# Kernel tuning notes

Measured on AMD Instinct MI355X. Metric: run time of the kernel, lower is better.

The kernel has to match this reference:

```python
import jax, jax.numpy as jnp
import numpy as np

D = 1024
B, S_IMG, S_CTX = 2, 4096, 512
EPS = 1e-6


def rmsnorm(x, eps=1e-6):
    return x * jax.lax.rsqrt(jnp.mean(x * x, axis=-1, keepdims=True) + eps)


def layernorm(x, eps=1e-6):
    mu = jnp.mean(x, axis=-1, keepdims=True)
    var = jnp.mean((x - mu) ** 2, axis=-1, keepdims=True)
    return (x - mu) * jax.lax.rsqrt(var + eps)


def act_quant(x):
    # per-token 8-bit absmax quant
    scale = 127.0 / jnp.clip(jnp.max(jnp.abs(x), axis=-1, keepdims=True), 1e-5)
    return jnp.clip(jnp.round(x * scale), -128, 127) / scale


def weight_quant(w):
    # ternary (1.58-bit) absmean quant
    scale = 1.0 / jnp.clip(jnp.mean(jnp.abs(w)), 1e-5)
    return jnp.clip(jnp.round(w * scale), -1, 1) / scale


def bitlinear(x, w):
    # BitNet: RMSNorm -> STE activation quant, STE ternary weight quant
    xn = rmsnorm(x)
    xq = xn + jax.lax.stop_gradient(act_quant(xn) - xn)
    wq = w + jax.lax.stop_gradient(weight_quant(w) - w)
    return jnp.einsum('bsd,od->bso', xq, wq)


def ada_ln_zero(x, emb, w, b):
    e = (jax.nn.silu(emb) @ w.T + b)[:, None, :]  # [B,1,6D]
    scale_msa, shift_msa, gate_msa, scale_mlp, shift_mlp, gate_mlp = jnp.split(e, 6, axis=2)
    xn = layernorm(x) * (1.0 + scale_msa) + shift_msa
    return xn, gate_msa, shift_mlp, scale_mlp, gate_mlp


def hgrn_bit_attention(x, wi, wf, wg, wo, gnorm_w):
    i = bitlinear(x, wi)
    f = jax.nn.sigmoid(bitlinear(x, wf))
    i = jax.nn.silu(i) * (1.0 - f)  # swiglu(i, 1-f)
    # elementwise linear recurrence h_t = f_t * h_{t-1} + i_t over seq dim
    def step(h, xs):
        i_t, f_t = xs
        h = f_t * h + i_t
        return h, h
    _, o = jax.lax.scan(step, jnp.zeros_like(i[:, 0]), (i.transpose(1, 0, 2), f.transpose(1, 0, 2)))
    o = o.transpose(1, 0, 2)  # [B,S,D]
    g = bitlinear(x, wg)
    o = rmsnorm(o) * gnorm_w * (g * jax.nn.sigmoid(g))  # RMSNorm + swish gate
    return bitlinear(o, wo)


def bit_mlp(x, w_gate, w_down):
    y = bitlinear(x, w_gate)
    gate, y = jnp.split(y, 2, axis=-1)
    return bitlinear(jax.nn.silu(gate) * y, w_down)


def flux_block(hidden_states, encoder_hidden_states, temb,
               adaln_w, adaln_b, adaln_ctx_w, adaln_ctx_b,
               attn_wi, attn_wf, attn_wg, attn_wo, attn_gnorm_w,
               ff_wgate, ff_wdown, ffc_wgate, ffc_wdown):
    nh, gate_msa, shift_mlp, scale_mlp, gate_mlp = ada_ln_zero(hidden_states, temb, adaln_w, adaln_b)
    nc, c_gate_msa, c_shift_mlp, c_scale_mlp, c_gate_mlp = ada_ln_zero(encoder_hidden_states, temb, adaln_ctx_w, adaln_ctx_b)
    len_c = nc.shape[1]
    joint = jnp.concatenate([nc, nh], axis=1)
    attn_out = hgrn_bit_attention(joint, attn_wi, attn_wf, attn_wg, attn_wo, attn_gnorm_w)
    c_attn, x_attn = attn_out[:, :len_c], attn_out[:, len_c:]

    hidden_states = hidden_states + gate_msa * x_attn
    nh2 = layernorm(hidden_states) * (1.0 + scale_mlp) + shift_mlp
    hidden_states = hidden_states + gate_mlp * bit_mlp(nh2, ff_wgate, ff_wdown)

    encoder_hidden_states = encoder_hidden_states + c_gate_msa * c_attn
    nc2 = layernorm(encoder_hidden_states) * (1.0 + c_scale_mlp) + c_shift_mlp
    encoder_hidden_states = encoder_hidden_states + c_gate_mlp * bit_mlp(nc2, ffc_wgate, ffc_wdown)
    return hidden_states, encoder_hidden_states


def setup_inputs() -> dict:
    key = jax.random.key(0)
    ks = jax.random.split(key, 16)
    w = lambda k, shape: jax.random.normal(k, shape, jnp.float32) * 0.02
    return {
        'hidden_states': jax.random.normal(ks[0], (B, S_IMG, D), jnp.float32),
        'encoder_hidden_states': jax.random.normal(ks[1], (B, S_CTX, D), jnp.float32),
        'temb': jax.random.normal(ks[2], (B, D), jnp.float32),
        'adaln_w': w(ks[3], (6 * D, D)), 'adaln_b': jnp.zeros((6 * D,), jnp.float32),
        'adaln_ctx_w': w(ks[4], (6 * D, D)), 'adaln_ctx_b': jnp.zeros((6 * D,), jnp.float32),
        'attn_wi': w(ks[5], (D, D)), 'attn_wf': w(ks[6], (D, D)),
        'attn_wg': w(ks[7], (D, D)), 'attn_wo': w(ks[8], (D, D)),
        'attn_gnorm_w': jnp.ones((D,), jnp.float32),
        'ff_wgate': w(ks[9], (8 * D, D)), 'ff_wdown': w(ks[10], (D, 4 * D)),
        'ffc_wgate': w(ks[11], (8 * D, D)), 'ffc_wdown': w(ks[12], (D, 4 * D)),
    }


def reference(hidden_states, encoder_hidden_states, temb,
              adaln_w, adaln_b, adaln_ctx_w, adaln_ctx_b,
              attn_wi, attn_wf, attn_wg, attn_wo, attn_gnorm_w,
              ff_wgate, ff_wdown, ffc_wgate, ffc_wdown):
    return flux_block(hidden_states, encoder_hidden_states, temb,
                      adaln_w, adaln_b, adaln_ctx_w, adaln_ctx_b,
                      attn_wi, attn_wf, attn_wg, attn_wo, attn_gnorm_w,
                      ff_wgate, ff_wdown, ffc_wgate, ffc_wdown)
```

## Files before the change

### kernel.cpp

```cpp
#include <hip/hip_runtime.h>
#include <hip/hip_bf16.h>
#include <stdint.h>

#define DM   1024
#define SJ   4608
#define SCTX 512
#define SIMG 4096
#define NCH  512
#define TCH  9

typedef __attribute__((ext_vector_type(4))) int   i32x4;
typedef __attribute__((ext_vector_type(4))) float f32x4;

__device__ __forceinline__ float bf2f(unsigned short u){
  union { unsigned int i; float f; } v; v.i = ((unsigned int)u) << 16; return v.f;
}
__device__ __forceinline__ unsigned short f2bf(float f){
  unsigned int u = __float_as_uint(f);
  u += 0x7fffu + ((u >> 16) & 1u);
  return (unsigned short)(u >> 16);
}
__device__ __forceinline__ float sigm(float x){ return 1.f/(1.f+__expf(-x)); }
__device__ __forceinline__ signed char q8(float v, float lo, float hi){
  return (signed char)(int)fminf(fmaxf(rintf(v),lo),hi);
}

__device__ __forceinline__ float wsum(float v){
  #pragma unroll
  for(int o=32;o>0;o>>=1) v += __shfl_xor(v,o);
  return v;
}
__device__ __forceinline__ float wmax(float v){
  #pragma unroll
  for(int o=32;o>0;o>>=1) v = fmaxf(v,__shfl_xor(v,o));
  return v;
}
__device__ __forceinline__ void blockSumSum(float& a, float& b, float* s1, float* s2){
  a = wsum(a); b = wsum(b);
  if(!(threadIdx.x&63)){ s1[threadIdx.x>>6]=a; s2[threadIdx.x>>6]=b; }
  __syncthreads();
  a = s1[0]+s1[1]+s1[2]+s1[3];
  b = s2[0]+s2[1]+s2[2]+s2[3];
  __syncthreads();
}
__device__ __forceinline__ void blockSumMax(float& a, float& b, float* s1, float* s2){
  a = wsum(a); b = wmax(b);
  if(!(threadIdx.x&63)){ s1[threadIdx.x>>6]=a; s2[threadIdx.x>>6]=b; }
  __syncthreads();
  a = s1[0]+s1[1]+s1[2]+s1[3];
  b = fmaxf(fmaxf(s2[0],s2[1]),fmaxf(s2[2],s2[3]));
  __syncthreads();
}

typedef __attribute__((address_space(1))) void gvoid_t;
typedef __attribute__((address_space(3))) void lvoid_t;
__device__ __forceinline__ void gl_lds16(const void* g, void* l){
  __builtin_amdgcn_global_load_lds((gvoid_t*)g, (lvoid_t*)l, 16, 0, 0);
}

struct WList {
  const float* w[8];
  unsigned long long n[8];
  signed char* q[8];
};

__global__ __launch_bounds__(256)
void wq_reduce(WList L, float* __restrict__ part){
  __shared__ float s1[4];
  int m = blockIdx.y;
  const float4* w4 = (const float4*)L.w[m];
  size_t n4 = L.n[m] >> 2;
  float s = 0.f;
  for(size_t i = (size_t)blockIdx.x*256 + threadIdx.x; i < n4; i += (size_t)512*256){
    float4 v = w4[i];
    s += fabsf(v.x)+fabsf(v.y)+fabsf(v.z)+fabsf(v.w);
  }
  s = wsum(s);
  if(!(threadIdx.x&63)) s1[threadIdx.x>>6] = s;
  __syncthreads();
  if(!threadIdx.x) part[m*512 + blockIdx.x] = s1[0]+s1[1]+s1[2]+s1[3];
}

__global__ __launch_bounds__(256)
void wq_finalize(WList L, const float* __restrict__ part, float* __restrict__ swinv){
  __shared__ float s1[4];
  int m = blockIdx.x;
  float s = part[m*512 + threadIdx.x] + part[m*512 + 256 + threadIdx.x];
  s = wsum(s);
  if(!(threadIdx.x&63)) s1[threadIdx.x>>6] = s;
  __syncthreads();
  if(!threadIdx.x){
    float mean = (s1[0]+s1[1]+s1[2]+s1[3]) / (float)L.n[m];
    swinv[m] = fmaxf(mean, 1e-5f);
  }
}

__global__ __launch_bounds__(256)
void wq_quant(WList L, const float* __restrict__ swinv){
  int m = blockIdx.y;
  float sc = 1.f / swinv[m];
  const float4* w4 = (const float4*)L.w[m];
  signed char* q = L.q[m];
  size_t n4 = L.n[m] >> 2;
  for(size_t i = (size_t)blockIdx.x*256 + threadIdx.x; i < n4; i += (size_t)1024*256){
    float4 v = w4[i];
    char4 o;
    o.x = q8(v.x*sc,-1.f,1.f);
    o.y = q8(v.y*sc,-1.f,1.f);
    o.z = q8(v.z*sc,-1.f,1.f);
    o.w = q8(v.w*sc,-1.f,1.f);
    ((char4*)q)[i] = o;
  }
}

__global__ __launch_bounds__(256)
void adaln_gemv(const float* __restrict__ temb, const float* __restrict__ W,
                const float* __restrict__ bias, float* __restrict__ e){
  int o = blockIdx.x*4 + (threadIdx.x>>6);
  int b = blockIdx.y;
  int lane = threadIdx.x & 63;
  const float4* t4 = (const float4*)(temb + b*DM);
  const float4* w4 = (const float4*)(W + (size_t)o*DM);
  float acc = 0.f;
  #pragma unroll
  for(int i=0;i<4;i++){
    float4 tv = t4[i*64+lane], wv = w4[i*64+lane];
    acc += (tv.x*sigm(tv.x))*wv.x + (tv.y*sigm(tv.y))*wv.y
         + (tv.z*sigm(tv.z))*wv.z + (tv.w*sigm(tv.w))*wv.w;
  }
  acc = wsum(acc);
  if(!lane) e[b*6144 + o] = acc + bias[o];
}

__global__ __launch_bounds__(256)
void modnorm_quant(const float* __restrict__ x, int bshift,
                   const float* __restrict__ e, int scaleOff, int shiftOff,
                   signed char* __restrict__ xq, float* __restrict__ rsx,
                   int outRowOff, int outBatchStride){
  __shared__ float s1[4], s2[4];
  const int tid = threadIdx.x;
  const int row = blockIdx.x;
  const int b = row >> bshift, s = row & ((1<<bshift)-1);
  float4 xv = ((const float4*)(x + (size_t)row*DM))[tid];
  float sum = xv.x+xv.y+xv.z+xv.w;
  float ss  = xv.x*xv.x+xv.y*xv.y+xv.z*xv.z+xv.w*xv.w;
  blockSumSum(sum, ss, s1, s2);
  float mu  = sum * (1.f/DM);
  float inv = rsqrtf(ss*(1.f/DM) - mu*mu + 1e-6f);
  float4 scv = ((const float4*)(e + b*6144 + scaleOff))[tid];
  float4 shv = ((const float4*)(e + b*6144 + shiftOff))[tid];
  float n0 = (xv.x-mu)*inv*(1.f+scv.x)+shv.x;
  float n1 = (xv.y-mu)*inv*(1.f+scv.y)+shv.y;
  float n2 = (xv.z-mu)*inv*(1.f+scv.z)+shv.z;
  float n3 = (xv.w-mu)*inv*(1.f+scv.w)+shv.w;
  float ss2 = n0*n0+n1*n1+n2*n2+n3*n3;
  float mx  = fmaxf(fmaxf(fabsf(n0),fabsf(n1)),fmaxf(fabsf(n2),fabsf(n3)));
  blockSumMax(ss2, mx, s1, s2);
  float rms   = rsqrtf(ss2*(1.f/DM) + 1e-6f);
  float amaxn = fmaxf(mx*rms, 1e-5f);
  float k     = rms*127.f/amaxn;
  int orow = b*outBatchStride + outRowOff + s;
  char4 q;
  q.x = q8(n0*k,-128.f,127.f);
  q.y = q8(n1*k,-128.f,127.f);
  q.z = q8(n2*k,-128.f,127.f);
  q.w = q8(n3*k,-128.f,127.f);
  ((char4*)(xq + (size_t)orow*DM))[tid] = q;
  if(!tid) rsx[orow] = amaxn*(1.f/127.f);
}

__global__ __launch_bounds__(256)
void resid_modnorm(const float* __restrict__ x, const unsigned short* __restrict__ attn,
                   int attnRowOff, int bshift,
                   const float* __restrict__ e,
                   float* __restrict__ hout,
                   signed char* __restrict__ xq, float* __restrict__ rsx){
  __shared__ float s1[4], s2[4];
  const int tid = threadIdx.x;
  const int row = blockIdx.x;
  const int b = row >> bshift, s = row & ((1<<bshift)-1);
  const int arow = b*SJ + attnRowOff + s;
  float4 xv = ((const float4*)(x + (size_t)row*DM))[tid];
  ushort4 av = ((const ushort4*)(attn + (size_t)arow*DM))[tid];
  float4 gv = ((const float4*)(e + b*6144 + 2*1024))[tid];
  float h0 = xv.x + gv.x*bf2f(av.x);
  float h1 = xv.y + gv.y*bf2f(av.y);
  float h2 = xv.z + gv.z*bf2f(av.z);
  float h3 = xv.w + gv.w*bf2f(av.w);
  ((float4*)(hout + (size_t)row*DM))[tid] = make_float4(h0,h1,h2,h3);
  float sum = h0+h1+h2+h3;
  float ss  = h0*h0+h1*h1+h2*h2+h3*h3;
  blockSumSum(sum, ss, s1, s2);
  float mu  = sum * (1.f/DM);
  float inv = rsqrtf(ss*(1.f/DM) - mu*mu + 1e-6f);
  float4 scv = ((const float4*)(e + b*6144 + 3*1024))[tid];
  float4 shv = ((const float4*)(e + b*6144 + 4*1024))[tid];
  float n0 = (h0-mu)*inv*(1.f+scv.x)+shv.x;
  float n1 = (h1-mu)*inv*(1.f+scv.y)+shv.y;
  float n2 = (h2-mu)*inv*(1.f+scv.z)+shv.z;
  float n3 = (h3-mu)*inv*(1.f+scv.w)+shv.w;
  float ss2 = n0*n0+n1*n1+n2*n2+n3*n3;
  float mx  = fmaxf(fmaxf(fabsf(n0),fabsf(n1)),fmaxf(fabsf(n2),fabsf(n3)));
  blockSumMax(ss2, mx, s1, s2);
  float rms   = rsqrtf(ss2*(1.f/DM) + 1e-6f);
  float amaxn = fmaxf(mx*rms, 1e-5f);
  float k     = rms*127.f/amaxn;
  char4 q;
  q.x = q8(n0*k,-128.f,127.f);
  q.y = q8(n1*k,-128.f,127.f);
  q.z = q8(n2*k,-128.f,127.f);
  q.w = q8(n3*k,-128.f,127.f);
  ((char4*)(xq + (size_t)row*DM))[tid] = q;
  if(!tid) rsx[row] = amaxn*(1.f/127.f);
}

__global__ __launch_bounds__(256)
void resid_out(const float* __restrict__ hnew, const unsigned short* __restrict__ mlp,
               const float* __restrict__ e, int bshift, float* __restrict__ out){
  const int tid = threadIdx.x;
  const int row = blockIdx.x;
  const int b = row >> bshift;
  float4 hv = ((const float4*)(hnew + (size_t)row*DM))[tid];
  ushort4 mv = ((const ushort4*)(mlp + (size_t)row*DM))[tid];
  float4 gv = ((const float4*)(e + b*6144 + 5*1024))[tid];
  float4 o;
  o.x = hv.x + gv.x*bf2f(mv.x);
  o.y = hv.y + gv.y*bf2f(mv.y);
  o.z = hv.z + gv.z*bf2f(mv.z);
  o.w = hv.w + gv.w*bf2f(mv.w);
  ((float4*)(out + (size_t)row*DM))[tid] = o;
}

__global__ __launch_bounds__(256)
void rmsq4096(const unsigned short* __restrict__ z, signed char* __restrict__ zq,
              float* __restrict__ rsx){
  __shared__ float s1[4], s2[4];
  const int tid = threadIdx.x;
  const unsigned short* zr = z + (size_t)blockIdx.x*4096;
  signed char* qr = zq + (size_t)blockIdx.x*4096;
  float v[16];
  #pragma unroll
  for(int i=0;i<4;i++){
    ushort4 u = ((const ushort4*)zr)[tid + i*256];
    v[i*4+0]=bf2f(u.x); v[i*4+1]=bf2f(u.y); v[i*4+2]=bf2f(u.z); v[i*4+3]=bf2f(u.w);
  }
  float ss=0.f, mx=0.f;
  #pragma unroll
  for(int i=0;i<16;i++){ ss += v[i]*v[i]; mx = fmaxf(mx, fabsf(v[i])); }
  blockSumMax(ss, mx, s1, s2);
  float rms   = rsqrtf(ss*(1.f/4096.f) + 1e-6f);
  float amaxn = fmaxf(mx*rms, 1e-5f);
  float k     = rms*127.f/amaxn;
  #pragma unroll
  for(int i=0;i<4;i++){
    char4 q;
    q.x = q8(v[i*4+0]*k,-128.f,127.f);
    q.y = q8(v[i*4+1]*k,-128.f,127.f);
    q.z = q8(v[i*4+2]*k,-128.f,127.f);
    q.w = q8(v[i*4+3]*k,-128.f,127.f);
    ((char4*)qr)[tid + i*256] = q;
  }
  if(!tid) rsx[blockIdx.x] = amaxn*(1.f/127.f);
}

__global__ __launch_bounds__(256)
void scan_pass1(const unsigned short* __restrict__ ir, const unsigned short* __restrict__ fr,
                float* __restrict__ A, float* __restrict__ B){
  int c = blockIdx.x, b = blockIdx.y;
  int d0 = threadIdx.x*4;
  size_t base = ((size_t)b*SJ + (size_t)c*TCH)*DM + d0;
  float a0=1,a1=1,a2=1,a3=1, h0=0,h1=0,h2=0,h3=0;
  #pragma unroll
  for(int t=0;t<TCH;t++){
    ushort4 iv = *(const ushort4*)(ir + base + (size_t)t*DM);
    ushort4 fv = *(const ushort4*)(fr + base + (size_t)t*DM);
    float f0=sigm(bf2f(fv.x)), f1=sigm(bf2f(fv.y)), f2=sigm(bf2f(fv.z)), f3=sigm(bf2f(fv.w));
    float x0=bf2f(iv.x), x1=bf2f(iv.y), x2=bf2f(iv.z), x3=bf2f(iv.w);
    float p0=x0*sigm(x0)*(1.f-f0), p1=x1*sigm(x1)*(1.f-f1);
    float p2=x2*sigm(x2)*(1.f-f2), p3=x3*sigm(x3)*(1.f-f3);
    h0=f0*h0+p0; h1=f1*h1+p1; h2=f2*h2+p2; h3=f3*h3+p3;
    a0*=f0; a1*=f1; a2*=f2; a3*=f3;
  }
  size_t idx = (size_t)c*2048 + b*1024 + d0;
  *(float4*)(A + idx) = make_float4(a0,a1,a2,a3);
  *(float4*)(B + idx) = make_float4(h0,h1,h2,h3);
}

__global__ __launch_bounds__(256)
void scan_pass2(const float* __restrict__ A, const float* __restrict__ B, float* __restrict__ H){
  int chain = blockIdx.x*256 + threadIdx.x;
  float h = 0.f;
  for(int c0=0;c0<NCH;c0+=8){
    float a[8], bb[8];
    #pragma unroll
    for(int u=0;u<8;u++){
      a[u]  = A[(size_t)(c0+u)*2048 + chain];
      bb[u] = B[(size_t)(c0+u)*2048 + chain];
    }
    #pragma unroll
    for(int u=0;u<8;u++){
      H[(size_t)(c0+u)*2048 + chain] = h;
      h = a[u]*h + bb[u];
    }
  }
}

__global__ __launch_bounds__(256)
void scan3_gnorm(const unsigned short* __restrict__ ir, const unsigned short* __restrict__ fr,
                 const float* __restrict__ H, const unsigned short* __restrict__ g,
                 const float* __restrict__ gnw,
                 signed char* __restrict__ xq, float* __restrict__ rsx){
  __shared__ float s1[4], s2[4];
  int c = blockIdx.x, b = blockIdx.y;
  const int tid = threadIdx.x;
  int d0 = tid*4;
  size_t base = ((size_t)b*SJ + (size_t)c*TCH)*DM + d0;
  float4 hv = *(const float4*)(H + (size_t)c*2048 + b*1024 + d0);
  float h0=hv.x, h1=hv.y, h2=hv.z, h3=hv.w;
  float4 wv = ((const float4*)gnw)[tid];
  #pragma unroll
  for(int t=0;t<TCH;t++){
    ushort4 iv = *(const ushort4*)(ir + base + (size_t)t*DM);
    ushort4 fv = *(const ushort4*)(fr + base + (size_t)t*DM);
    float f0=sigm(bf2f(fv.x)), f1=sigm(bf2f(fv.y)), f2=sigm(bf2f(fv.z)), f3=sigm(bf2f(fv.w));
    float x0=bf2f(iv.x), x1=bf2f(iv.y), x2=bf2f(iv.z), x3=bf2f(iv.w);
    float p0=x0*sigm(x0)*(1.f-f0), p1=x1*sigm(x1)*(1.f-f1);
    float p2=x2*sigm(x2)*(1.f-f2), p3=x3*sigm(x3)*(1.f-f3);
    h0=f0*h0+p0; h1=f1*h1+p1; h2=f2*h2+p2; h3=f3*h3+p3;
    float ss = h0*h0+h1*h1+h2*h2+h3*h3, dummy = 0.f;
    blockSumSum(ss, dummy, s1, s2);
    float rms = rsqrtf(ss*(1.f/DM) + 1e-6f);
    ushort4 gv = *(const ushort4*)(g + base + (size_t)t*DM);
    float g0=bf2f(gv.x), g1=bf2f(gv.y), g2=bf2f(gv.z), g3=bf2f(gv.w);
    float n0 = h0*rms*wv.x*(g0*sigm(g0));
    float n1 = h1*rms*wv.y*(g1*sigm(g1));
    float n2 = h2*rms*wv.z*(g2*sigm(g2));
    float n3 = h3*rms*wv.w*(g3*sigm(g3));
    float ss2 = n0*n0+n1*n1+n2*n2+n3*n3;
    float mx  = fmaxf(fmaxf(fabsf(n0),fabsf(n1)),fmaxf(fabsf(n2),fabsf(n3)));
    blockSumMax(ss2, mx, s1, s2);
    float rms2  = rsqrtf(ss2*(1.f/DM) + 1e-6f);
    float amaxn = fmaxf(mx*rms2, 1e-5f);
    float k     = rms2*127.f/amaxn;
    char4 q;
    q.x = q8(n0*k,-128.f,127.f);
    q.y = q8(n1*k,-128.f,127.f);
    q.z = q8(n2*k,-128.f,127.f);
    q.w = q8(n3*k,-128.f,127.f);
    size_t row = (size_t)b*SJ + (size_t)c*TCH + t;
    *(char4*)(xq + row*DM + d0) = q;
    if(!tid) rsx[row] = amaxn*(1.f/127.f);
  }
}

#define EPI_IFG    0
#define EPI_OUT    1
#define EPI_GLU    2

struct GemmP {
  const float* rsx;
  const float* swinv;
  unsigned short* outb;
  float* outf;
  const float* egate;
  int bshift;
  const signed char* w2;
};

template<int VAR, int EPI, int SWZ>
__global__ __launch_bounds__(512, 2)
void gemm8(const signed char* __restrict__ Aq, const signed char* __restrict__ Bq,
           int Ncols, int K, int lda, GemmP p){
  constexpr int BBYT = (VAR==2)? 16384 : 32768;
  constexpr int TB   = 32768 + BBYT;
  constexpr int NF   = (VAR==0)? 4 : 2;
  constexpr int BN   = (VAR==0)? 256 : 128;
  __shared__ char lds[2*TB];

  const int tid = threadIdx.x, wv = tid>>6, lane = tid&63;
  const int wm = wv>>2, wn = wv&3;
  const int nwg = gridDim.x*gridDim.y;
  const int id  = blockIdx.y*gridDim.x + blockIdx.x;
  int nb, mb;
  if constexpr (SWZ==1){
    const int x = id&7, j = id>>3;
    nb = x*4 + (j&3);
    mb = j>>2;
  } else {
    const int wg = (id&7)*(nwg>>3) + (id>>3);
    nb = wg % gridDim.x; mb = wg / gridDim.x;
  }

  const int srow = wv*8 + (lane>>3);
  const int sch  = ((lane&7) ^ (lane>>3))*16;
  const signed char* ag  = Aq + (size_t)(mb*256 + srow)*lda + sch;
  const signed char* bg1 = Bq + (size_t)(nb*BN  + srow)*lda + sch;
  const signed char* bg2 = nullptr;
  if constexpr (VAR==1) bg2 = p.w2 + (size_t)(nb*128 + srow)*lda + sch;
  const int wvoff = wv*1024;

  auto stageA = [&](char* bufn, int rb, int k0){
    gl_lds16(ag + (size_t)rb*lda + k0, bufn + rb*128 + wvoff);
  };
  auto stageB = [&](char* bufn, int rb, int k0, int m2){
    const signed char* src = m2 ? bg2 : bg1;
    gl_lds16(src + (size_t)rb*lda + k0, bufn + 32768 + m2*16384 + rb*128 + wvoff);
  };
  auto stagePh = [&](int ph, char* bufn, int kn){
    if constexpr (VAR==0){
      if(ph==0){ stageB(bufn,0,kn,0);   stageB(bufn,64,kn,0); }
      else if(ph==1){ stageB(bufn,128,kn,0); stageB(bufn,192,kn,0); }
      else if(ph==2){ stageA(bufn,0,kn);   stageA(bufn,128,kn); }
      else          { stageA(bufn,64,kn);  stageA(bufn,192,kn); }
    } else if constexpr (VAR==1){
      if(ph==0){ stageB(bufn,0,kn,0);  stageB(bufn,64,kn,0); }
      else if(ph==1){ stageB(bufn,0,kn,1);  stageB(bufn,64,kn,1); }
      else if(ph==2){ stageA(bufn,0,kn);   stageA(bufn,128,kn); }
      else          { stageA(bufn,64,kn);  stageA(bufn,192,kn); }
    } else {
      if(ph==0){ stageB(bufn,0,kn,0);  stageB(bufn,64,kn,0); }
      else if(ph==1){ stageA(bufn,0,kn);   stageA(bufn,128,kn); }
      else if(ph==2){ stageA(bufn,64,kn);  stageA(bufn,192,kn); }
    }
  };

  const int lr = lane&15;
  const int kq = lane>>4;
  const int axor = (lr&7)<<4;
  const int col0 = (kq<<4) ^ axor;
  const int col1 = (64 | (kq<<4)) ^ axor;
  const int arowb = (wm*128 + lr)*128;
  const int browb = ((VAR==0? wn*64 : wn*32) + lr)*128;

  i32x4 acc[8][NF];
  i32x4 acc2[(VAR==1)?8:1][NF];
  #pragma unroll
  for(int i=0;i<8;i++)
    #pragma unroll
    for(int j=0;j<NF;j++){ acc[i][j]=(i32x4){0,0,0,0}; if constexpr(VAR==1) acc2[i][j]=(i32x4){0,0,0,0}; }

  i32x4 breg[NF], breg2[(VAR==1)?NF:1];

  auto phase = [&](char* bufc, int ph, char* bufn, int kn, bool doStage){
    const int colb = (ph>>1)? col1 : col0;
    const int mh = ph&1;
    if(mh==0){
      #pragma unroll
      for(int nf=0;nf<NF;nf++)
        breg[nf] = *(const i32x4*)(bufc + 32768 + browb + nf*2048 + colb);
      if constexpr (VAR==1){
        #pragma unroll
        for(int nf=0;nf<NF;nf++)
          breg2[nf] = *(const i32x4*)(bufc + 32768 + 16384 + browb + nf*2048 + colb);
      }
    }
    i32x4 areg[4];
    #pragma unroll
    for(int i=0;i<4;i++)
      areg[i] = *(const i32x4*)(bufc + arowb + (mh*4+i)*2048 + colb);
    if(doStage) stagePh(ph, bufn, kn);
    __builtin_amdgcn_s_setprio(1);
    #pragma unroll
    for(int i=0;i<4;i++){
      #pragma unroll
      for(int nf=0;nf<NF;nf++){
        acc[mh*4+i][nf] = __builtin_amdgcn_mfma_i32_16x16x64_i8(areg[i], breg[nf], acc[mh*4+i][nf], 0,0,0);
        if constexpr (VAR==1)
          acc2[mh*4+i][nf] = __builtin_amdgcn_mfma_i32_16x16x64_i8(areg[i], breg2[nf], acc2[mh*4+i][nf], 0,0,0);
      }
    }
    __builtin_amdgcn_s_setprio(0);
  };

  #define VMW2 asm volatile("s_waitcnt vmcnt(2)" ::: "memory")
  #define VMW0 asm volatile("s_waitcnt vmcnt(0)" ::: "memory")
  #define BARR { __builtin_amdgcn_s_barrier(); __builtin_amdgcn_sched_barrier(0); }

  stagePh(0, lds, 0); stagePh(1, lds, 0); stagePh(2, lds, 0); stagePh(3, lds, 0);

  const int NT = K>>7;
  for(int t=0; t<NT-1; ++t){
    char* bufc = lds + (t&1)*TB;
    char* bufn = lds + ((t+1)&1)*TB;
    const int kn = (t+1)<<7;
    VMW2; BARR; phase(bufc, 0, bufn, kn, true);
    VMW2; BARR; phase(bufc, 1, bufn, kn, true);
          BARR; phase(bufc, 2, bufn, kn, true);
          BARR; phase(bufc, 3, bufn, kn, true);
  }
  {
    char* bufc = lds + ((NT-1)&1)*TB;
    VMW2; BARR; phase(bufc, 0, nullptr, 0, false);
    VMW0; BARR; phase(bufc, 1, nullptr, 0, false);
          BARR; phase(bufc, 2, nullptr, 0, false);
          BARR; phase(bufc, 3, nullptr, 0, false);
  }

  float sw;
  if constexpr (EPI==EPI_IFG) sw = p.swinv[(nb*256)>>10];
  else                        sw = *p.swinv;
  const int r0 = mb*256 + wm*128;
  const int c0 = nb*BN + wn*((VAR==0)?64:32);
  #pragma unroll
  for(int mf=0;mf<8;mf++){
    #pragma unroll
    for(int j=0;j<4;j++){
      int r = r0 + mf*16 + kq*4 + j;
      float rs = p.rsx[r]*sw;
      #pragma unroll
      for(int nf=0;nf<NF;nf++){
        int c = c0 + nf*16 + lr;
        float val = (float)acc[mf][nf][j]*rs;
        if constexpr (EPI==EPI_IFG){
          int mat = c >> 10;
          p.outb[(size_t)mat*9437184 + (size_t)r*1024 + (c&1023)] = f2bf(val);
        } else if constexpr (EPI==EPI_GLU){
          float v2 = (float)acc2[mf][nf][j]*rs;
          p.outb[(size_t)r*Ncols + c] = f2bf(val*sigm(val)*v2);
        } else {
          p.outb[(size_t)r*Ncols + c] = f2bf(val);
        }
      }
    }
  }
  #undef VMW2
  #undef VMW0
  #undef BARR
}

__global__ __launch_bounds__(256, 2)
void gemm_ra8(const signed char* __restrict__ Aq, const signed char* __restrict__ Wq,
              int K, int lda, GemmP p){
  __shared__ signed char As[128*128];
  __shared__ signed char Bs[128*128];
  const int tid = threadIdx.x;
  const int wave = tid>>6, lane = tid&63;
  const int nwg = gridDim.x*gridDim.y;
  const int id  = blockIdx.y*gridDim.x + blockIdx.x;
  const int wg  = (id&7)*(nwg>>3) + (id>>3);
  const int nb  = wg % gridDim.x, mb = wg / gridDim.x;
  const int wr = wave>>1, wc = wave&1;
  const int koff = blockIdx.z*K;

  const int grow = wave*8 + (lane>>3);
  const int gcol = (lane&7)*16;
  const signed char* ag = Aq + (size_t)(mb*128 + grow)*lda + koff + gcol;
  const signed char* bg = Wq + (size_t)(nb*128 + grow)*lda + koff + gcol;
  char* asl = (char*)As + wave*1024;
  char* bsl = (char*)Bs + wave*1024;

  i32x4 acc[4][4];
  #pragma unroll
  for(int i=0;i<4;i++)
    #pragma unroll
    for(int j=0;j<4;j++) acc[i][j] = (i32x4){0,0,0,0};

  const int lrow = lane&15, kq = lane>>4;
  const signed char* arow = &As[(wr*64 + lrow)*128 + kq*16];
  const signed char* brow = &Bs[(wc*64 + lrow)*128 + kq*16];

  for(int k0=0; k0<K; k0+=128){
    #pragma unroll
    for(int pp=0;pp<4;pp++){
      gl_lds16(ag + (size_t)pp*32*lda + k0, asl + pp*4096);
      gl_lds16(bg + (size_t)pp*32*lda + k0, bsl + pp*4096);
    }
    __syncthreads();
    #pragma unroll
    for(int kk=0;kk<2;kk++){
      i32x4 af[4], bfr[4];
      #pragma unroll
      for(int m=0;m<4;m++) af[m]  = *(const i32x4*)(arow + m*2048 + kk*64);
      #pragma unroll
      for(int n=0;n<4;n++) bfr[n] = *(const i32x4*)(brow + n*2048 + kk*64);
      #pragma unroll
      for(int m=0;m<4;m++)
        #pragma unroll
        for(int n=0;n<4;n++)
          acc[m][n] = __builtin_amdgcn_mfma_i32_16x16x64_i8(af[m], bfr[n], acc[m][n], 0,0,0);
    }
    __syncthreads();
  }

  const float sw = *p.swinv;
  const int r0 = mb*128 + wr*64, c0 = nb*128 + wc*64;
  #pragma unroll
  for(int m=0;m<4;m++){
    #pragma unroll
    for(int j=0;j<4;j++){
      int r = r0 + m*16 + kq*4 + j;
      float rs = p.rsx[r]*sw;
      #pragma unroll
      for(int n=0;n<4;n++){
        int c = c0 + n*16 + lrow;
        float val = (float)acc[m][n][j]*rs;
        int b = r >> p.bshift;
        size_t idx = (size_t)r*DM + c;
        atomicAdd(&p.outf[idx], p.egate[b*6144 + 5*1024 + c]*val);
      }
    }
  }
}

extern "C" void kernel_launch(void* const* d_in, const int* in_sizes, int n_in,
                              void* d_out, int out_size, void* d_ws, size_t ws_size,
                              hipStream_t stream){
  (void)in_sizes; (void)n_in; (void)out_size; (void)ws_size;
  const float* hidden   = (const float*)d_in[0];
  const float* enc      = (const float*)d_in[1];
  const float* temb     = (const float*)d_in[2];
  const float* adaln_w  = (const float*)d_in[3];
  const float* adaln_b  = (const float*)d_in[4];
  const float* adaln_cw = (const float*)d_in[5];
  const float* adaln_cb = (const float*)d_in[6];
  const float* wi  = (const float*)d_in[7];
  const float* wf  = (const float*)d_in[8];
  const float* wg  = (const float*)d_in[9];
  const float* wo  = (const float*)d_in[10];
  const float* gnw = (const float*)d_in[11];
  const float* ffg = (const float*)d_in[12];
  const float* ffd = (const float*)d_in[13];
  const float* fcg = (const float*)d_in[14];
  const float* fcd = (const float*)d_in[15];

  const size_t MB = 1024ull*1024ull;
  char* ws = (char*)d_ws;
  signed char* W8_IFG = (signed char*)(ws + 0*MB);
  signed char* W8_WO  = (signed char*)(ws + 3*MB);
  signed char* W8_FFG = (signed char*)(ws + 4*MB);
  signed char* W8_FFD = (signed char*)(ws + 12*MB);
  signed char* W8_FCG = (signed char*)(ws + 16*MB);
  signed char* W8_FCD = (signed char*)(ws + 24*MB);
  float* PART  = (float*)(ws + 28*MB);
  float* SWINV = (float*)(ws + 28*MB + 32*1024);
  float* EH    = (float*)(ws + 28*MB + 64*1024);
  float* EC    = (float*)(ws + 28*MB + 112*1024);
  float* RSX1  = (float*)(ws + 28*MB + 160*1024);
  float* RSX2  = (float*)(ws + 28*MB + 200*1024);
  float* RSX3  = (float*)(ws + 28*MB + 240*1024);
  float* RSXZ  = (float*)(ws + 28*MB + 280*1024);
  float* RSX4  = (float*)(ws + 28*MB + 320*1024);
  float* RSXZC = (float*)(ws + 28*MB + 328*1024);
  float* SCANA = (float*)(ws + 29*MB);
  float* SCANB = (float*)(ws + 33*MB);
  float* SCANH = (float*)(ws + 37*MB);
  signed char* XQ8 = (signed char*)(ws + 41*MB);
  unsigned short* IRAW = (unsigned short*)(ws + 51*MB);
  unsigned short* FRAW = (unsigned short*)(ws + 69*MB);
  unsigned short* GRAW = (unsigned short*)(ws + 87*MB);
  unsigned short* ATTN = (unsigned short*)(ws + 51*MB);
  signed char* SG8 = (signed char*)(ws + 51*MB);
  unsigned short* MLPH = (unsigned short*)(ws + 83*MB);
  float* HNEW = (float*)(ws + 105*MB);
  unsigned short* SGB = (unsigned short*)(ws + 137*MB);
  float* OUT_H = (float*)d_out;
  float* OUT_C = (float*)d_out + 8388608;

  WList L;
  L.w[0]=wi;  L.n[0]=1048576ull; L.q[0]=W8_IFG;
  L.w[1]=wf;  L.n[1]=1048576ull; L.q[1]=W8_IFG + 1048576;
  L.w[2]=wg;  L.n[2]=1048576ull; L.q[2]=W8_IFG + 2097152;
  L.w[3]=wo;  L.n[3]=1048576ull; L.q[3]=W8_WO;
  L.w[4]=ffg; L.n[4]=8388608ull; L.q[4]=W8_FFG;
  L.w[5]=ffd; L.n[5]=4194304ull; L.q[5]=W8_FFD;
  L.w[6]=fcg; L.n[6]=8388608ull; L.q[6]=W8_FCG;
  L.w[7]=fcd; L.n[7]=4194304ull; L.q[7]=W8_FCD;
  wq_reduce  <<<dim3(512,8), 256, 0, stream>>>(L, PART);
  wq_finalize<<<8,          256, 0, stream>>>(L, PART, SWINV);
  wq_quant   <<<dim3(1024,8),256, 0, stream>>>(L, SWINV);

  adaln_gemv<<<dim3(1536,2), 256, 0, stream>>>(temb, adaln_w,  adaln_b,  EH);
  adaln_gemv<<<dim3(1536,2), 256, 0, stream>>>(temb, adaln_cw, adaln_cb, EC);

  modnorm_quant<<<1024, 256, 0, stream>>>(enc,    9,  EC, 0, 1024, XQ8, RSX1, 0,   SJ);
  modnorm_quant<<<8192, 256, 0, stream>>>(hidden, 12, EH, 0, 1024, XQ8, RSX1, 512, SJ);

  GemmP p{};
  p.rsx = RSX1; p.swinv = SWINV; p.outb = IRAW;
  gemm8<0,EPI_IFG,0><<<dim3(12,36), 512, 0, stream>>>(XQ8, W8_IFG, 3072, 1024, 1024, p);

  scan_pass1<<<dim3(NCH,2), 256, 0, stream>>>(IRAW, FRAW, SCANA, SCANB);
  scan_pass2<<<8,           256, 0, stream>>>(SCANA, SCANB, SCANH);
  scan3_gnorm<<<dim3(NCH,2), 256, 0, stream>>>(IRAW, FRAW, SCANH, GRAW, gnw, XQ8, RSX2);

  GemmP pw{};
  pw.rsx = RSX2; pw.swinv = SWINV+3; pw.outb = ATTN;
  gemm8<2,EPI_OUT,0><<<dim3(8,36), 512, 0, stream>>>(XQ8, W8_WO, 1024, 1024, 1024, pw);

  resid_modnorm<<<8192, 256, 0, stream>>>(hidden, ATTN, 512, 12, EH, HNEW, XQ8, RSX3);
  resid_modnorm<<<1024, 256, 0, stream>>>(enc,    ATTN, 0,   9,  EC, OUT_C,
                                          XQ8 + (size_t)8192*1024, RSX4);

  GemmP pg{};
  pg.rsx = RSX3; pg.swinv = SWINV+4; pg.outb = SGB; pg.w2 = W8_FFG + (size_t)4096*1024;
  gemm8<1,EPI_GLU,1><<<dim3(32,32), 512, 0, stream>>>(XQ8, W8_FFG, 4096, 1024, 1024, pg);
  rmsq4096<<<8192, 256, 0, stream>>>(SGB, SG8, RSXZ);
  GemmP pd{};
  pd.rsx = RSXZ; pd.swinv = SWINV+5; pd.outb = MLPH;
  gemm8<2,EPI_OUT,0><<<dim3(8,32), 512, 0, stream>>>(SG8, W8_FFD, 1024, 4096, 4096, pd);
  resid_out<<<8192, 256, 0, stream>>>(HNEW, MLPH, EH, 12, OUT_H);

  GemmP pc{};
  pc.rsx = RSX4; pc.swinv = SWINV+6; pc.outb = SGB; pc.w2 = W8_FCG + (size_t)4096*1024;
  gemm8<1,EPI_GLU,1><<<dim3(32,4), 512, 0, stream>>>(XQ8 + (size_t)8192*1024, W8_FCG, 4096, 1024, 1024, pc);
  rmsq4096<<<1024, 256, 0, stream>>>(SGB, SG8, RSXZC);
  GemmP pe{};
  pe.rsx = RSXZC; pe.swinv = SWINV+7; pe.outf = OUT_C; pe.egate = EC; pe.bshift = 9;
  gemm_ra8<<<dim3(8,8,4), 256, 0, stream>>>(SG8, W8_FCD, 1024, 4096, pe);
}
```

Baseline: 465.4 us.

## Software-pipeline LDS fragment reads one phase ahead in int8 GEMM main loop

Restructures the int8 MFMA GEMM main loop so the A/B fragments for the next phase are read from LDS while the current phase's MFMAs run, using double register sets (aS0/aS1, bA/bB). Global-to-LDS staging is regrouped into two larger bursts per K-tile instead of four small ones. The aim is to hide LDS read latency behind MFMA execution and cut the stalls caused by reading fragments right before use. In exchange it needs more VGPRs for the extra fragment registers, which may hurt occupancy at 2 waves/SIMD, and the barrier/waitcnt ordering is more delicate.

```diff
diff --git a/kernel.cpp b/kernel.cpp
--- a/kernel.cpp
+++ b/kernel.cpp
@@ -375,6 +375,7 @@
   constexpr int TB   = 32768 + BBYT;
   constexpr int NF   = (VAR==0)? 4 : 2;
   constexpr int BN   = (VAR==0)? 256 : 128;
+  constexpr int NBF  = (VAR==1)? 2*NF : NF;
   __shared__ char lds[2*TB];
 
   const int tid = threadIdx.x, wv = tid>>6, lane = tid&63;
@@ -406,21 +407,20 @@
     const signed char* src = m2 ? bg2 : bg1;
     gl_lds16(src + (size_t)rb*lda + k0, bufn + 32768 + m2*16384 + rb*128 + wvoff);
   };
-  auto stagePh = [&](int ph, char* bufn, int kn){
+  auto stage_p0 = [&](char* bufn, int kn){
     if constexpr (VAR==0){
-      if(ph==0){ stageB(bufn,0,kn,0);   stageB(bufn,64,kn,0); }
-      else if(ph==1){ stageB(bufn,128,kn,0); stageB(bufn,192,kn,0); }
-      else if(ph==2){ stageA(bufn,0,kn);   stageA(bufn,128,kn); }
-      else          { stageA(bufn,64,kn);  stageA(bufn,192,kn); }
+      stageB(bufn,0,kn,0); stageB(bufn,64,kn,0); stageB(bufn,128,kn,0); stageB(bufn,192,kn,0);
     } else if constexpr (VAR==1){
-      if(ph==0){ stageB(bufn,0,kn,0);  stageB(bufn,64,kn,0); }
-      else if(ph==1){ stageB(bufn,0,kn,1);  stageB(bufn,64,kn,1); }
-      else if(ph==2){ stageA(bufn,0,kn);   stageA(bufn,128,kn); }
-      else          { stageA(bufn,64,kn);  stageA(bufn,192,kn); }
+      stageB(bufn,0,kn,0); stageB(bufn,64,kn,0); stageB(bufn,0,kn,1); stageB(bufn,64,kn,1);
     } else {
-      if(ph==0){ stageB(bufn,0,kn,0);  stageB(bufn,64,kn,0); }
-      else if(ph==1){ stageA(bufn,0,kn);   stageA(bufn,128,kn); }
-      else if(ph==2){ stageA(bufn,64,kn);  stageA(bufn,192,kn); }
+      stageB(bufn,0,kn,0); stageB(bufn,64,kn,0); stageA(bufn,0,kn); stageA(bufn,128,kn);
+    }
+  };
+  auto stage_p1 = [&](char* bufn, int kn){
+    if constexpr (VAR==2){
+      stageA(bufn,64,kn); stageA(bufn,192,kn);
+    } else {
+      stageA(bufn,0,kn); stageA(bufn,128,kn); stageA(bufn,64,kn); stageA(bufn,192,kn);
     }
   };
 
@@ -439,34 +439,32 @@
     #pragma unroll
     for(int j=0;j<NF;j++){ acc[i][j]=(i32x4){0,0,0,0}; if constexpr(VAR==1) acc2[i][j]=(i32x4){0,0,0,0}; }
 
-  i32x4 breg[NF], breg2[(VAR==1)?NF:1];
-
-  auto phase = [&](char* bufc, int ph, char* bufn, int kn, bool doStage){
-    const int colb = (ph>>1)? col1 : col0;
-    const int mh = ph&1;
-    if(mh==0){
+  i32x4 aS0[4], aS1[4], bA[NBF], bB[NBF];
+
+  auto readA = [&](i32x4* d, const char* buf, int colb, int mh){
+    #pragma unroll
+    for(int i=0;i<4;i++)
+      d[i] = *(const i32x4*)(buf + arowb + (mh*4+i)*2048 + colb);
+  };
+  auto readB = [&](i32x4* d, const char* buf, int colb){
+    #pragma unroll
+    for(int nf=0;nf<NF;nf++)
+      d[nf] = *(const i32x4*)(buf + 32768 + browb + nf*2048 + colb);
+    if constexpr (VAR==1){
       #pragma unroll
       for(int nf=0;nf<NF;nf++)
-        breg[nf] = *(const i32x4*)(bufc + 32768 + browb + nf*2048 + colb);
-      if constexpr (VAR==1){
-        #pragma unroll
-        for(int nf=0;nf<NF;nf++)
-          breg2[nf] = *(const i32x4*)(bufc + 32768 + 16384 + browb + nf*2048 + colb);
-      }
-    }
-    i32x4 areg[4];
-    #pragma unroll
-    for(int i=0;i<4;i++)
-      areg[i] = *(const i32x4*)(bufc + arowb + (mh*4+i)*2048 + colb);
-    if(doStage) stagePh(ph, bufn, kn);
+        d[NF+nf] = *(const i32x4*)(buf + 32768 + 16384 + browb + nf*2048 + colb);
+    }
+  };
+  auto mfmaPh = [&](int mh, const i32x4* ar, const i32x4* br){
     __builtin_amdgcn_s_setprio(1);
     #pragma unroll
     for(int i=0;i<4;i++){
       #pragma unroll
       for(int nf=0;nf<NF;nf++){
-        acc[mh*4+i][nf] = __builtin_amdgcn_mfma_i32_16x16x64_i8(areg[i], breg[nf], acc[mh*4+i][nf], 0,0,0);
+        acc[mh*4+i][nf] = __builtin_amdgcn_mfma_i32_16x16x64_i8(ar[i], br[nf], acc[mh*4+i][nf], 0,0,0);
         if constexpr (VAR==1)
-          acc2[mh*4+i][nf] = __builtin_amdgcn_mfma_i32_16x16x64_i8(areg[i], breg2[nf], acc2[mh*4+i][nf], 0,0,0);
+          acc2[mh*4+i][nf] = __builtin_amdgcn_mfma_i32_16x16x64_i8(ar[i], br[NF+nf], acc2[mh*4+i][nf], 0,0,0);
       }
     }
     __builtin_amdgcn_s_setprio(0);
@@ -474,26 +472,48 @@
 
   #define VMW2 asm volatile("s_waitcnt vmcnt(2)" ::: "memory")
   #define VMW0 asm volatile("s_waitcnt vmcnt(0)" ::: "memory")
-  #define BARR { __builtin_amdgcn_s_barrier(); __builtin_amdgcn_sched_barrier(0); }
-
-  stagePh(0, lds, 0); stagePh(1, lds, 0); stagePh(2, lds, 0); stagePh(3, lds, 0);
+  #define SYNC1 { __builtin_amdgcn_s_barrier(); \
+                  asm volatile("s_waitcnt lgkmcnt(0)" ::: "memory"); \
+                  __builtin_amdgcn_sched_barrier(0); }
+  #define SYNC2 { __builtin_amdgcn_s_barrier(); }
+
+  stage_p0(lds, 0);
+  stage_p1(lds, 0);
+  VMW0;
+  __builtin_amdgcn_s_barrier();
+  readB(bA, lds, col0);
+  readA(aS0, lds, col0, 0);
 
   const int NT = K>>7;
   for(int t=0; t<NT-1; ++t){
     char* bufc = lds + (t&1)*TB;
     char* bufn = lds + ((t+1)&1)*TB;
     const int kn = (t+1)<<7;
-    VMW2; BARR; phase(bufc, 0, bufn, kn, true);
-    VMW2; BARR; phase(bufc, 1, bufn, kn, true);
-          BARR; phase(bufc, 2, bufn, kn, true);
-          BARR; phase(bufc, 3, bufn, kn, true);
+    readA(aS1, bufc, col0, 1);
+    stage_p0(bufn, kn);
+    SYNC1; mfmaPh(0, aS0, bA); SYNC2;
+    readB(bB, bufc, col1);
+    readA(aS0, bufc, col1, 0);
+    stage_p1(bufn, kn);
+    SYNC1; mfmaPh(1, aS1, bA); SYNC2;
+    readA(aS1, bufc, col1, 1);
+    VMW2;
+    SYNC1; mfmaPh(0, aS0, bB); SYNC2;
+    readB(bA, bufn, col0);
+    readA(aS0, bufn, col0, 0);
+    VMW0;
+    SYNC1; mfmaPh(1, aS1, bB); SYNC2;
   }
   {
     char* bufc = lds + ((NT-1)&1)*TB;
-    VMW2; BARR; phase(bufc, 0, nullptr, 0, false);
-    VMW0; BARR; phase(bufc, 1, nullptr, 0, false);
-          BARR; phase(bufc, 2, nullptr, 0, false);
-          BARR; phase(bufc, 3, nullptr, 0, false);
+    readA(aS1, bufc, col0, 1);
+    SYNC1; mfmaPh(0, aS0, bA); SYNC2;
+    readB(bB, bufc, col1);
+    readA(aS0, bufc, col1, 0);
+    SYNC1; mfmaPh(1, aS1, bA); SYNC2;
+    readA(aS1, bufc, col1, 1);
+    SYNC1; mfmaPh(0, aS0, bB); SYNC2;
+    mfmaPh(1, aS1, bB);
   }
 
   float sw;
@@ -525,7 +545,8 @@
   }
   #undef VMW2
   #undef VMW0
-  #undef BARR
+  #undef SYNC1
+  #undef SYNC2
 }
 
 __global__ __launch_bounds__(256, 2)
```

After: 485.6 us. 1.04x slower.

## Shrink int8 GEMM tiles to 128 rows, 4 waves, K-step 64 with simpler pipeline

Applied to the files above, without the earlier changes.

The int8 MFMA GEMM moves from 512-thread blocks with 256-row tiles and a four-phase, 128-deep K pipeline to 256-thread blocks with 128-row tiles and a single-phase double-buffered loop over K-steps of 64. The grid doubles in M so more workgroups exist, and LDS per block drops. The goal is better occupancy and simpler synchronization, at the cost of lower data reuse per tile, more barriers per K, and less fine-grained overlap of loads with MFMA.

```diff
diff --git a/kernel.cpp b/kernel.cpp
--- a/kernel.cpp
+++ b/kernel.cpp
@@ -367,18 +367,26 @@
   const signed char* w2;
 };
 
+template<int N>
+__device__ __forceinline__ void vm_wait(){
+  if constexpr(N==0)      asm volatile("s_waitcnt vmcnt(0)" ::: "memory");
+  else if constexpr(N==4) asm volatile("s_waitcnt vmcnt(4)" ::: "memory");
+  else                    asm volatile("s_waitcnt vmcnt(6)" ::: "memory");
+}
+
 template<int VAR, int EPI, int SWZ>
-__global__ __launch_bounds__(512, 2)
+__global__ __launch_bounds__(256, 2)
 void gemm8(const signed char* __restrict__ Aq, const signed char* __restrict__ Bq,
            int Ncols, int K, int lda, GemmP p){
-  constexpr int BBYT = (VAR==2)? 16384 : 32768;
-  constexpr int TB   = 32768 + BBYT;
+  constexpr int BN   = (VAR==0)? 256 : 128;
   constexpr int NF   = (VAR==0)? 4 : 2;
-  constexpr int BN   = (VAR==0)? 256 : 128;
+  constexpr int NBF  = (VAR==1)? 4 : NF;
+  constexpr int BH   = (VAR==0)? 128 : 64;
+  constexpr int TB   = (VAR==2)? 16384 : 24576;
+  constexpr int NC   = (VAR==2)? 4 : 6;
   __shared__ char lds[2*TB];
 
-  const int tid = threadIdx.x, wv = tid>>6, lane = tid&63;
-  const int wm = wv>>2, wn = wv&3;
+  const int tid = threadIdx.x, wn = tid>>6, lane = tid&63;
   const int nwg = gridDim.x*gridDim.y;
   const int id  = blockIdx.y*gridDim.x + blockIdx.x;
   int nb, mb;
@@ -391,46 +399,58 @@
     nb = wg % gridDim.x; mb = wg / gridDim.x;
   }
 
-  const int srow = wv*8 + (lane>>3);
-  const int sch  = ((lane&7) ^ (lane>>3))*16;
-  const signed char* ag  = Aq + (size_t)(mb*256 + srow)*lda + sch;
-  const signed char* bg1 = Bq + (size_t)(nb*BN  + srow)*lda + sch;
-  const signed char* bg2 = nullptr;
-  if constexpr (VAR==1) bg2 = p.w2 + (size_t)(nb*128 + srow)*lda + sch;
-  const int wvoff = wv*1024;
-
-  auto stageA = [&](char* bufn, int rb, int k0){
-    gl_lds16(ag + (size_t)rb*lda + k0, bufn + rb*128 + wvoff);
+  const int sl = tid>>3;
+  const int sd = (tid&7) ^ (sl&7);
+  const int sdk = (sd&3)*16;
+  const int sdh = sd>>2;
+  const signed char* agp  = Aq + (size_t)(mb*128 + sl + sdh*64)*lda + sdk;
+  const signed char* bg1p = Bq + (size_t)(nb*BN  + sl + sdh*BH)*lda + sdk;
+  const signed char* bg2p = nullptr;
+  if constexpr (VAR==1) bg2p = p.w2 + (size_t)(nb*128 + sl + sdh*64)*lda + sdk;
+
+  auto stage = [&](char* buf, int k0){
+    gl_lds16(agp + k0,           buf + tid*16);
+    gl_lds16(agp + 32*lda + k0,  buf + 4096 + tid*16);
+    if constexpr (VAR==0){
+      gl_lds16(bg1p + k0,           buf + 8192  + tid*16);
+      gl_lds16(bg1p + 32*lda + k0,  buf + 12288 + tid*16);
+      gl_lds16(bg1p + 64*lda + k0,  buf + 16384 + tid*16);
+      gl_lds16(bg1p + 96*lda + k0,  buf + 20480 + tid*16);
+    } else if constexpr (VAR==1){
+      gl_lds16(bg1p + k0,           buf + 8192  + tid*16);
+      gl_lds16(bg1p + 32*lda + k0,  buf + 12288 + tid*16);
+      gl_lds16(bg2p + k0,           buf + 16384 + tid*16);
+      gl_lds16(bg2p + 32*lda + k0,  buf + 20480 + tid*16);
+    } else {
+      gl_lds16(bg1p + k0,           buf + 8192  + tid*16);
+      gl_lds16(bg1p + 32*lda + k0,  buf + 12288 + tid*16);
+    }
   };
-  auto stageB = [&](char* bufn, int rb, int k0, int m2){
-    const signed char* src = m2 ? bg2 : bg1;
-    gl_lds16(src + (size_t)rb*lda + k0, bufn + 32768 + m2*16384 + rb*128 + wvoff);
-  };
-  auto stagePh = [&](int ph, char* bufn, int kn){
-    if constexpr (VAR==0){
-      if(ph==0){ stageB(bufn,0,kn,0);   stageB(bufn,64,kn,0); }
-      else if(ph==1){ stageB(bufn,128,kn,0); stageB(bufn,192,kn,0); }
-      else if(ph==2){ stageA(bufn,0,kn);   stageA(bufn,128,kn); }
-      else          { stageA(bufn,64,kn);  stageA(bufn,192,kn); }
-    } else if constexpr (VAR==1){
-      if(ph==0){ stageB(bufn,0,kn,0);  stageB(bufn,64,kn,0); }
-      else if(ph==1){ stageB(bufn,0,kn,1);  stageB(bufn,64,kn,1); }
-      else if(ph==2){ stageA(bufn,0,kn);   stageA(bufn,128,kn); }
-      else          { stageA(bufn,64,kn);  stageA(bufn,192,kn); }
-    } else {
-      if(ph==0){ stageB(bufn,0,kn,0);  stageB(bufn,64,kn,0); }
-      else if(ph==1){ stageA(bufn,0,kn);   stageA(bufn,128,kn); }
-      else if(ph==2){ stageA(bufn,64,kn);  stageA(bufn,192,kn); }
-    }
-  };
-
-  const int lr = lane&15;
-  const int kq = lane>>4;
-  const int axor = (lr&7)<<4;
-  const int col0 = (kq<<4) ^ axor;
-  const int col1 = (64 | (kq<<4)) ^ axor;
-  const int arowb = (wm*128 + lr)*128;
-  const int browb = ((VAR==0? wn*64 : wn*32) + lr)*128;
+
+  const int lr = lane&15, kq = lane>>4;
+  int aoff[8];
+  #pragma unroll
+  for(int mf=0;mf<8;mf++){
+    int R = mf*16 + lr;
+    aoff[mf] = (R&63)*128 + ((((R>>6)<<2)|kq) ^ (R&7))*16;
+  }
+  int boff[NBF];
+  if constexpr (VAR==0){
+    #pragma unroll
+    for(int nf=0;nf<4;nf++){
+      int RB = wn*64 + nf*16 + lr;
+      boff[nf] = 8192 + (RB&127)*128 + ((((RB>>7)<<2)|kq) ^ (RB&7))*16;
+    }
+  } else {
+    #pragma unroll
+    for(int m=0;m<((VAR==1)?2:1);m++){
+      #pragma unroll
+      for(int nf=0;nf<2;nf++){
+        int RB = wn*32 + nf*16 + lr;
+        boff[m*2+nf] = 8192 + m*8192 + (RB&63)*128 + ((((RB>>6)<<2)|kq) ^ (RB&7))*16;
+      }
+    }
+  }
 
   i32x4 acc[8][NF];
   i32x4 acc2[(VAR==1)?8:1][NF];
@@ -439,67 +459,48 @@
     #pragma unroll
     for(int j=0;j<NF;j++){ acc[i][j]=(i32x4){0,0,0,0}; if constexpr(VAR==1) acc2[i][j]=(i32x4){0,0,0,0}; }
 
-  i32x4 breg[NF], breg2[(VAR==1)?NF:1];
-
-  auto phase = [&](char* bufc, int ph, char* bufn, int kn, bool doStage){
-    const int colb = (ph>>1)? col1 : col0;
-    const int mh = ph&1;
-    if(mh==0){
-      #pragma unroll
-      for(int nf=0;nf<NF;nf++)
-        breg[nf] = *(const i32x4*)(bufc + 32768 + browb + nf*2048 + colb);
-      if constexpr (VAR==1){
-        #pragma unroll
-        for(int nf=0;nf<NF;nf++)
-          breg2[nf] = *(const i32x4*)(bufc + 32768 + 16384 + browb + nf*2048 + colb);
-      }
-    }
-    i32x4 areg[4];
-    #pragma unroll
-    for(int i=0;i<4;i++)
-      areg[i] = *(const i32x4*)(bufc + arowb + (mh*4+i)*2048 + colb);
-    if(doStage) stagePh(ph, bufn, kn);
-    __builtin_amdgcn_s_setprio(1);
-    #pragma unroll
-    for(int i=0;i<4;i++){
+  auto tileBody = [&](const char* buf){
+    i32x4 af[8], bf_[NBF];
+    #pragma unroll
+    for(int mf=0;mf<8;mf++) af[mf] = *(const i32x4*)(buf + aoff[mf]);
+    #pragma unroll
+    for(int q=0;q<NBF;q++)  bf_[q] = *(const i32x4*)(buf + boff[q]);
+    #pragma unroll
+    for(int mf=0;mf<8;mf++){
       #pragma unroll
       for(int nf=0;nf<NF;nf++){
-        acc[mh*4+i][nf] = __builtin_amdgcn_mfma_i32_16x16x64_i8(areg[i], breg[nf], acc[mh*4+i][nf], 0,0,0);
+        acc[mf][nf] = __builtin_amdgcn_mfma_i32_16x16x64_i8(af[mf], bf_[nf], acc[mf][nf], 0,0,0);
         if constexpr (VAR==1)
-          acc2[mh*4+i][nf] = __builtin_amdgcn_mfma_i32_16x16x64_i8(areg[i], breg2[nf], acc2[mh*4+i][nf], 0,0,0);
+          acc2[mf][nf] = __builtin_amdgcn_mfma_i32_16x16x64_i8(af[mf], bf_[NF+nf], acc2[mf][nf], 0,0,0);
       }
     }
-    __builtin_amdgcn_s_setprio(0);
   };
 
-  #define VMW2 asm volatile("s_waitcnt vmcnt(2)" ::: "memory")
-  #define VMW0 asm volatile("s_waitcnt vmcnt(0)" ::: "memory")
-  #define BARR { __builtin_amdgcn_s_barrier(); __builtin_amdgcn_sched_barrier(0); }
-
-  stagePh(0, lds, 0); stagePh(1, lds, 0); stagePh(2, lds, 0); stagePh(3, lds, 0);
-
-  const int NT = K>>7;
+  stage(lds, 0);
+  const int NT = K>>6;
   for(int t=0; t<NT-1; ++t){
     char* bufc = lds + (t&1)*TB;
     char* bufn = lds + ((t+1)&1)*TB;
-    const int kn = (t+1)<<7;
-    VMW2; BARR; phase(bufc, 0, bufn, kn, true);
-    VMW2; BARR; phase(bufc, 1, bufn, kn, true);
-          BARR; phase(bufc, 2, bufn, kn, true);
-          BARR; phase(bufc, 3, bufn, kn, true);
+    stage(bufn, (t+1)<<6);
+    vm_wait<NC>();
+    __builtin_amdgcn_s_barrier();
+    __builtin_amdgcn_sched_barrier(0);
+    tileBody(bufc);
+    __builtin_amdgcn_sched_barrier(0);
+    __builtin_amdgcn_s_barrier();
   }
   {
     char* bufc = lds + ((NT-1)&1)*TB;
-    VMW2; BARR; phase(bufc, 0, nullptr, 0, false);
-    VMW0; BARR; phase(bufc, 1, nullptr, 0, false);
-          BARR; phase(bufc, 2, nullptr, 0, false);
-          BARR; phase(bufc, 3, nullptr, 0, false);
+    vm_wait<0>();
+    __builtin_amdgcn_s_barrier();
+    __builtin_amdgcn_sched_barrier(0);
+    tileBody(bufc);
   }
 
   float sw;
-  if constexpr (EPI==EPI_IFG) sw = p.swinv[(nb*256)>>10];
+  if constexpr (EPI==EPI_IFG) sw = p.swinv[(nb*BN)>>10];
   else                        sw = *p.swinv;
-  const int r0 = mb*256 + wm*128;
+  const int r0 = mb*128;
   const int c0 = nb*BN + wn*((VAR==0)?64:32);
   #pragma unroll
   for(int mf=0;mf<8;mf++){
@@ -523,9 +524,6 @@
       }
     }
   }
-  #undef VMW2
-  #undef VMW0
-  #undef BARR
 }
 
 __global__ __launch_bounds__(256, 2)
@@ -677,7 +675,7 @@
 
   GemmP p{};
   p.rsx = RSX1; p.swinv = SWINV; p.outb = IRAW;
-  gemm8<0,EPI_IFG,0><<<dim3(12,36), 512, 0, stream>>>(XQ8, W8_IFG, 3072, 1024, 1024, p);
+  gemm8<0,EPI_IFG,0><<<dim3(12,72), 256, 0, stream>>>(XQ8, W8_IFG, 3072, 1024, 1024, p);
 
   scan_pass1<<<dim3(NCH,2), 256, 0, stream>>>(IRAW, FRAW, SCANA, SCANB);
   scan_pass2<<<8,           256, 0, stream>>>(SCANA, SCANB, SCANH);
@@ -685,7 +683,7 @@
 
   GemmP pw{};
   pw.rsx = RSX2; pw.swinv = SWINV+3; pw.outb = ATTN;
-  gemm8<2,EPI_OUT,0><<<dim3(8,36), 512, 0, stream>>>(XQ8, W8_WO, 1024, 1024, 1024, pw);
+  gemm8<2,EPI_OUT,0><<<dim3(8,72), 256, 0, stream>>>(XQ8, W8_WO, 1024, 1024, 1024, pw);
 
   resid_modnorm<<<8192, 256, 0, stream>>>(hidden, ATTN, 512, 12, EH, HNEW, XQ8, RSX3);
   resid_modnorm<<<1024, 256, 0, stream>>>(enc,    ATTN, 0,   9,  EC, OUT_C,
@@ -693,16 +691,16 @@
 
   GemmP pg{};
   pg.rsx = RSX3; pg.swinv = SWINV+4; pg.outb = SGB; pg.w2 = W8_FFG + (size_t)4096*1024;
-  gemm8<1,EPI_GLU,1><<<dim3(32,32), 512, 0, stream>>>(XQ8, W8_FFG, 4096, 1024, 1024, pg);
+  gemm8<1,EPI_GLU,1><<<dim3(32,64), 256, 0, stream>>>(XQ8, W8_FFG, 4096, 1024, 1024, pg);
   rmsq4096<<<8192, 256, 0, stream>>>(SGB, SG8, RSXZ);
   GemmP pd{};
   pd.rsx = RSXZ; pd.swinv = SWINV+5; pd.outb = MLPH;
-  gemm8<2,EPI_OUT,0><<<dim3(8,32), 512, 0, stream>>>(SG8, W8_FFD, 1024, 4096, 4096, pd);
+  gemm8<2,EPI_OUT,0><<<dim3(8,64), 256, 0, stream>>>(SG8, W8_FFD, 1024, 4096, 4096, pd);
   resid_out<<<8192, 256, 0, stream>>>(HNEW, MLPH, EH, 12, OUT_H);
 
   GemmP pc{};
   pc.rsx = RSX4; pc.swinv = SWINV+6; pc.outb = SGB; pc.w2 = W8_FCG + (size_t)4096*1024;
-  gemm8<1,EPI_GLU,1><<<dim3(32,4), 512, 0, stream>>>(XQ8 + (size_t)8192*1024, W8_FCG, 4096, 1024, 1024, pc);
+  gemm8<1,EPI_GLU,1><<<dim3(32,8), 256, 0, stream>>>(XQ8 + (size_t)8192*1024, W8_FCG, 4096, 1024, 1024, pc);
   rmsq4096<<<1024, 256, 0, stream>>>(SGB, SG8, RSXZC);
   GemmP pe{};
   pe.rsx = RSXZC; pe.swinv = SWINV+7; pe.outf = OUT_C; pe.egate = EC; pe.bshift = 9;
```

New measurement: 472.1 us. No clear change (+1.4%).
